# Kernel optimization log

Measured on AMD Instinct MI355X. Metric: run time of the kernel, lower is better.

The kernel has to match this reference:

```python
import jax, jax.numpy as jnp
import numpy as np

B, T, D, H = 2, 2048, 768, 12
HD = D // H  # head_dim = 64


def setup_inputs() -> dict:
    key = jax.random.key(0)
    ks = jax.random.split(key, 10)
    s = 0.02
    return {
        "hidden_states": jax.random.normal(ks[0], (B, T, D), jnp.float32),
        "attention_mask": jnp.zeros((B, 1, T, T), jnp.float32),
        "relative_position_bias": jax.random.normal(ks[1], (H, T, T), jnp.float32) * s,
        "Wq": jax.random.normal(ks[2], (D, D), jnp.float32) * s,
        "bq": jnp.zeros((D,), jnp.float32),
        "Wk": jax.random.normal(ks[3], (D, D), jnp.float32) * s,
        "bk": jnp.zeros((D,), jnp.float32),
        "Wv": jax.random.normal(ks[4], (D, D), jnp.float32) * s,
        "bv": jnp.zeros((D,), jnp.float32),
        "Wo": jax.random.normal(ks[5], (D, D), jnp.float32) * s,
        "bo": jnp.zeros((D,), jnp.float32),
    }


def reference(hidden_states, attention_mask, relative_position_bias,
              Wq, bq, Wk, bk, Wv, bv, Wo, bo):
    b, t, d = hidden_states.shape
    scale = HD ** -0.5
    # projections (nn.Linear: x @ W^T + b)
    q = (hidden_states @ Wq.T + bq) * scale
    k = hidden_states @ Wk.T + bk
    v = hidden_states @ Wv.T + bv
    # [b, h, t, hd]
    q = q.reshape(b, t, H, HD).transpose(0, 2, 1, 3)
    k = k.reshape(b, t, H, HD).transpose(0, 2, 1, 3)
    v = v.reshape(b, t, H, HD).transpose(0, 2, 1, 3)
    # scores: [b, h, t, s]
    attn = jnp.einsum("bhtd,bhsd->bhts", q, k)
    attn = attn + relative_position_bias[None, :, :, :]
    attn = attn + attention_mask  # (b,1,t,s) broadcast over heads
    attn = jax.nn.softmax(attn, axis=-1)
    out = jnp.einsum("bhts,bhsd->bhtd", attn, v)
    out = out.transpose(0, 2, 1, 3).reshape(b, t, d)
    return out @ Wo.T + bo
```

## Files before the change

kernel.cpp:

```cpp
#include <hip/hip_runtime.h>
#include <hip/hip_bf16.h>

#define B_  2
#define T_  2048
#define D_  768
#define H_  12
#define HD_ 64

typedef short bf16x8 __attribute__((ext_vector_type(8)));
typedef float f32x4  __attribute__((ext_vector_type(4)));

static __device__ __forceinline__ unsigned short f2bf(float f) {
    union { float f; unsigned u; } v; v.f = f;
    unsigned r = (v.u + 0x7FFFu + ((v.u >> 16) & 1u)) >> 16;
    return (unsigned short)r;
}

__global__ void cvt_f32_bf16(const float* __restrict__ in,
                             unsigned short* __restrict__ out, int n8) {
    int i = blockIdx.x * blockDim.x + threadIdx.x;
    int stride = gridDim.x * blockDim.x;
    for (; i < n8; i += stride) {
        float4 a = *(const float4*)(in + (size_t)i * 8);
        float4 b = *(const float4*)(in + (size_t)i * 8 + 4);
        union { unsigned short s[8]; int4 v; } o;
        o.s[0] = f2bf(a.x); o.s[1] = f2bf(a.y); o.s[2] = f2bf(a.z); o.s[3] = f2bf(a.w);
        o.s[4] = f2bf(b.x); o.s[5] = f2bf(b.y); o.s[6] = f2bf(b.z); o.s[7] = f2bf(b.w);
        *(int4*)(out + (size_t)i * 8) = o.v;
    }
}

__global__ __launch_bounds__(256)
void gemm_bt_bf16(const unsigned short* __restrict__ A,
                  const unsigned short* __restrict__ Bw,
                  const float* __restrict__ bias,
                  void* __restrict__ out, float scale, int mode)
{
    __shared__ __align__(16) unsigned short As[128 * 40];
    __shared__ __align__(16) unsigned short Bs[128 * 40];

    const int tid  = threadIdx.x;
    const int lane = tid & 63;
    const int wid  = tid >> 6;
    const int wm   = wid >> 1, wn = wid & 1;
    const int l15  = lane & 15, l16 = lane >> 4;
    const int bm   = blockIdx.x * 128, bn = blockIdx.y * 128;

    f32x4 acc[4][4];
    #pragma unroll
    for (int mi = 0; mi < 4; ++mi)
        #pragma unroll
        for (int ni = 0; ni < 4; ++ni)
            acc[mi][ni] = (f32x4){0.f, 0.f, 0.f, 0.f};

    const int r0 = tid >> 2,          o0 = (tid & 3) * 8;
    const int r1 = (tid + 256) >> 2,  o1 = ((tid + 256) & 3) * 8;

    for (int k0 = 0; k0 < 768; k0 += 32) {
        int4 a0 = *(const int4*)(A  + (size_t)(bm + r0) * 768 + k0 + o0);
        int4 a1 = *(const int4*)(A  + (size_t)(bm + r1) * 768 + k0 + o1);
        int4 b0 = *(const int4*)(Bw + (size_t)(bn + r0) * 768 + k0 + o0);
        int4 b1 = *(const int4*)(Bw + (size_t)(bn + r1) * 768 + k0 + o1);
        *(int4*)(As + r0 * 40 + o0) = a0;
        *(int4*)(As + r1 * 40 + o1) = a1;
        *(int4*)(Bs + r0 * 40 + o0) = b0;
        *(int4*)(Bs + r1 * 40 + o1) = b1;
        __syncthreads();

        bf16x8 af[4], bf[4];
        #pragma unroll
        for (int mi = 0; mi < 4; ++mi)
            af[mi] = *(const bf16x8*)(As + (wm * 64 + mi * 16 + l15) * 40 + l16 * 8);
        #pragma unroll
        for (int ni = 0; ni < 4; ++ni)
            bf[ni] = *(const bf16x8*)(Bs + (wn * 64 + ni * 16 + l15) * 40 + l16 * 8);
        #pragma unroll
        for (int mi = 0; mi < 4; ++mi)
            #pragma unroll
            for (int ni = 0; ni < 4; ++ni)
                acc[mi][ni] = __builtin_amdgcn_mfma_f32_16x16x32_bf16(
                    af[mi], bf[ni], acc[mi][ni], 0, 0, 0);
        __syncthreads();
    }

    if (mode == 0) {
        float* o = (float*)out;
        #pragma unroll
        for (int ni = 0; ni < 4; ++ni) {
            int col = bn + wn * 64 + ni * 16 + l15;
            float bv = bias[col];
            #pragma unroll
            for (int mi = 0; mi < 4; ++mi)
                #pragma unroll
                for (int reg = 0; reg < 4; ++reg) {
                    int row = bm + wm * 64 + mi * 16 + l16 * 4 + reg;
                    o[(size_t)row * 768 + col] = acc[mi][ni][reg] + bv;
                }
        }
    } else {
        unsigned short* o = (unsigned short*)out;
        #pragma unroll
        for (int ni = 0; ni < 4; ++ni) {
            int col = bn + wn * 64 + ni * 16 + l15;
            float bv = bias[col];
            int h = col >> 6, hd = col & 63;
            #pragma unroll
            for (int mi = 0; mi < 4; ++mi)
                #pragma unroll
                for (int reg = 0; reg < 4; ++reg) {
                    int row = bm + wm * 64 + mi * 16 + l16 * 4 + reg;
                    int bb = row >> 11, t = row & (T_ - 1);
                    float v = (acc[mi][ni][reg] + bv) * scale;
                    o[(((size_t)bb * H_ + h) * T_ + t) * HD_ + hd] = f2bf(v);
                }
        }
    }
}

__global__ __launch_bounds__(256)
void attn_fwd_mfma(const unsigned short* __restrict__ q,
                   const unsigned short* __restrict__ k,
                   const unsigned short* __restrict__ v,
                   const float* __restrict__ bias,
                   const float* __restrict__ mask,
                   unsigned short* __restrict__ ctx)
{
    __shared__ __align__(16) unsigned short Ks[64 * 72];
    __shared__ __align__(16) unsigned short Vt[64 * 72];
    __shared__ __align__(16) unsigned short Ps[64 * 72];

    const int tid  = threadIdx.x;
    const int lane = tid & 63;
    const int wq   = tid >> 6;
    const int l15  = lane & 15, l16 = lane >> 4;
    const int bh   = blockIdx.y;
    const int b    = bh / H_, h = bh % H_;
    const int q0   = blockIdx.x * 64;

    const unsigned short* qb = q + (size_t)bh * T_ * HD_;
    const unsigned short* kb = k + (size_t)bh * T_ * HD_;
    const unsigned short* vb = v + (size_t)bh * T_ * HD_;

    bf16x8 qf[2];
    {
        const unsigned short* qp = qb + (size_t)(q0 + wq * 16 + l15) * HD_;
        qf[0] = *(const bf16x8*)(qp + l16 * 8);
        qf[1] = *(const bf16x8*)(qp + 32 + l16 * 8);
    }

    float m_run[4], l_run[4];
    f32x4 o[4];
    #pragma unroll
    for (int r = 0; r < 4; ++r) {
        m_run[r] = -3.0e38f; l_run[r] = 0.f;
        o[r] = (f32x4){0.f, 0.f, 0.f, 0.f};
    }

    const size_t brow = (size_t)h * T_ * T_ + (size_t)(q0 + wq * 16) * T_;
    const size_t mrow = (size_t)b * T_ * T_ + (size_t)(q0 + wq * 16) * T_;

    for (int s0 = 0; s0 < T_; s0 += 64) {
        #pragma unroll
        for (int it = 0; it < 2; ++it) {
            int slot = tid + it * 256;
            int row = slot >> 3, c8 = (slot & 7) * 8;
            int4 kv = *(const int4*)(kb + (size_t)(s0 + row) * HD_ + c8);
            *(int4*)(Ks + row * 72 + c8) = kv;
            int key = slot & 63, hd0 = (slot >> 6) * 8;
            int4 vv = *(const int4*)(vb + (size_t)(s0 + key) * HD_ + hd0);
            const unsigned short* vs = (const unsigned short*)&vv;
            #pragma unroll
            for (int e = 0; e < 8; ++e)
                Vt[(hd0 + e) * 72 + key] = vs[e];
        }
        __syncthreads();

        float badd[4][4];
        #pragma unroll
        for (int f = 0; f < 4; ++f)
            #pragma unroll
            for (int reg = 0; reg < 4; ++reg) {
                size_t off = (size_t)(l16 * 4 + reg) * T_ + s0 + f * 16 + l15;
                badd[f][reg] = bias[brow + off] + mask[mrow + off];
            }

        f32x4 s[4];
        #pragma unroll
        for (int f = 0; f < 4; ++f) {
            bf16x8 k0f = *(const bf16x8*)(Ks + (f * 16 + l15) * 72 + l16 * 8);
            bf16x8 k1f = *(const bf16x8*)(Ks + (f * 16 + l15) * 72 + 32 + l16 * 8);
            f32x4 t = (f32x4){0.f, 0.f, 0.f, 0.f};
            t = __builtin_amdgcn_mfma_f32_16x16x32_bf16(qf[0], k0f, t, 0, 0, 0);
            t = __builtin_amdgcn_mfma_f32_16x16x32_bf16(qf[1], k1f, t, 0, 0, 0);
            s[f] = t;
        }

        #pragma unroll
        for (int f = 0; f < 4; ++f)
            #pragma unroll
            for (int reg = 0; reg < 4; ++reg)
                s[f][reg] += badd[f][reg];

        float sc[4];
        #pragma unroll
        for (int reg = 0; reg < 4; ++reg) {
            float mx = fmaxf(fmaxf(s[0][reg], s[1][reg]), fmaxf(s[2][reg], s[3][reg]));
            #pragma unroll
            for (int off = 1; off < 16; off <<= 1)
                mx = fmaxf(mx, __shfl_xor(mx, off));
            float m_new = fmaxf(m_run[reg], mx);
            float scv = __expf(m_run[reg] - m_new);
            float ssum = 0.f;
            #pragma unroll
            for (int f = 0; f < 4; ++f) {
                float p = __expf(s[f][reg] - m_new);
                s[f][reg] = p; ssum += p;
            }
            #pragma unroll
            for (int off = 1; off < 16; off <<= 1)
                ssum += __shfl_xor(ssum, off);
            l_run[reg] = l_run[reg] * scv + ssum;
            m_run[reg] = m_new;
            sc[reg] = scv;
        }
        #pragma unroll
        for (int f = 0; f < 4; ++f)
            #pragma unroll
            for (int reg = 0; reg < 4; ++reg)
                o[f][reg] *= sc[reg];

        unsigned short* Pw = Ps + wq * 16 * 72;
        #pragma unroll
        for (int f = 0; f < 4; ++f)
            #pragma unroll
            for (int reg = 0; reg < 4; ++reg)
                Pw[(l16 * 4 + reg) * 72 + f * 16 + l15] = f2bf(s[f][reg]);

        #pragma unroll
        for (int kc = 0; kc < 2; ++kc) {
            bf16x8 pf = *(const bf16x8*)(Pw + l15 * 72 + kc * 32 + l16 * 8);
            #pragma unroll
            for (int f = 0; f < 4; ++f) {
                bf16x8 vf = *(const bf16x8*)(Vt + (f * 16 + l15) * 72 + kc * 32 + l16 * 8);
                o[f] = __builtin_amdgcn_mfma_f32_16x16x32_bf16(pf, vf, o[f], 0, 0, 0);
            }
        }
        __syncthreads();
    }

    unsigned short* cb = ctx + ((size_t)b * T_ + q0 + wq * 16) * D_ + h * HD_;
    #pragma unroll
    for (int reg = 0; reg < 4; ++reg) {
        float inv = 1.f / l_run[reg];
        int r = l16 * 4 + reg;
        #pragma unroll
        for (int f = 0; f < 4; ++f)
            cb[(size_t)r * D_ + f * 16 + l15] = f2bf(o[f][reg] * inv);
    }
}

extern "C" void kernel_launch(void* const* d_in, const int* in_sizes, int n_in,
                              void* d_out, int out_size, void* d_ws, size_t ws_size,
                              hipStream_t stream) {
    const float* hs   = (const float*)d_in[0];
    const float* mask = (const float*)d_in[1];
    const float* bias = (const float*)d_in[2];
    const float* Wq   = (const float*)d_in[3];
    const float* bq   = (const float*)d_in[4];
    const float* Wk   = (const float*)d_in[5];
    const float* bk   = (const float*)d_in[6];
    const float* Wv   = (const float*)d_in[7];
    const float* bv   = (const float*)d_in[8];
    const float* Wo   = (const float*)d_in[9];
    const float* bo   = (const float*)d_in[10];
    float* out = (float*)d_out;

    const size_t NE = (size_t)B_ * T_ * D_;
    const size_t WE = (size_t)D_ * D_;
    unsigned short* ws = (unsigned short*)d_ws;
    unsigned short* hs_bf = ws;
    unsigned short* Wq_bf = hs_bf + NE;
    unsigned short* Wk_bf = Wq_bf + WE;
    unsigned short* Wv_bf = Wk_bf + WE;
    unsigned short* Wo_bf = Wv_bf + WE;
    unsigned short* qw    = Wo_bf + WE;
    unsigned short* kw    = qw + NE;
    unsigned short* vw    = kw + NE;
    unsigned short* ctxb  = vw + NE;

    {
        int n8 = (int)(NE / 8);
        cvt_f32_bf16<<<dim3((n8 + 255) / 256 > 2048 ? 2048 : (n8 + 255) / 256), 256, 0, stream>>>(hs, hs_bf, n8);
        int w8 = (int)(WE / 8);
        dim3 wg((w8 + 255) / 256);
        cvt_f32_bf16<<<wg, 256, 0, stream>>>(Wq, Wq_bf, w8);
        cvt_f32_bf16<<<wg, 256, 0, stream>>>(Wk, Wk_bf, w8);
        cvt_f32_bf16<<<wg, 256, 0, stream>>>(Wv, Wv_bf, w8);
        cvt_f32_bf16<<<wg, 256, 0, stream>>>(Wo, Wo_bf, w8);
    }

    dim3 ggrid(32, 6);
    const float scale = 0.125f;
    gemm_bt_bf16<<<ggrid, 256, 0, stream>>>(hs_bf, Wq_bf, bq, qw, scale, 1);
    gemm_bt_bf16<<<ggrid, 256, 0, stream>>>(hs_bf, Wk_bf, bk, kw, 1.0f, 1);
    gemm_bt_bf16<<<ggrid, 256, 0, stream>>>(hs_bf, Wv_bf, bv, vw, 1.0f, 1);

    attn_fwd_mfma<<<dim3(T_ / 64, B_ * H_), 256, 0, stream>>>(qw, kw, vw, bias, mask, ctxb);

    gemm_bt_bf16<<<ggrid, 256, 0, stream>>>(ctxb, Wo_bf, bo, out, 1.0f, 0);
}
```

Before: 479.6 us.

## Fuse QKV GEMMs, batch weight casts, use direct-to-LDS loads, transpose score layout

```diff
diff --git a/kernel.cpp b/kernel.cpp
--- a/kernel.cpp
+++ b/kernel.cpp
@@ -1,5 +1,4 @@
 #include <hip/hip_runtime.h>
-#include <hip/hip_bf16.h>
 
 #define B_  2
 #define T_  2048
@@ -9,6 +8,7 @@
 
 typedef short bf16x8 __attribute__((ext_vector_type(8)));
 typedef float f32x4  __attribute__((ext_vector_type(4)));
+typedef unsigned int u32;
 
 static __device__ __forceinline__ unsigned short f2bf(float f) {
     union { float f; unsigned u; } v; v.f = f;
@@ -30,80 +30,96 @@
     }
 }
 
+__global__ void cvt_weights(const float* __restrict__ w0, const float* __restrict__ w1,
+                            const float* __restrict__ w2, const float* __restrict__ w3,
+                            unsigned short* __restrict__ out, int n8) {
+    const float* src = (blockIdx.y == 0) ? w0 : (blockIdx.y == 1) ? w1
+                     : (blockIdx.y == 2) ? w2 : w3;
+    unsigned short* dst = out + (size_t)blockIdx.y * (D_ * D_);
+    int i = blockIdx.x * blockDim.x + threadIdx.x;
+    int stride = gridDim.x * blockDim.x;
+    for (; i < n8; i += stride) {
+        float4 a = *(const float4*)(src + (size_t)i * 8);
+        float4 b = *(const float4*)(src + (size_t)i * 8 + 4);
+        union { unsigned short s[8]; int4 v; } o;
+        o.s[0] = f2bf(a.x); o.s[1] = f2bf(a.y); o.s[2] = f2bf(a.z); o.s[3] = f2bf(a.w);
+        o.s[4] = f2bf(b.x); o.s[5] = f2bf(b.y); o.s[6] = f2bf(b.z); o.s[7] = f2bf(b.w);
+        *(int4*)(dst + (size_t)i * 8) = o.v;
+    }
+}
+
 __global__ __launch_bounds__(256)
-void gemm_bt_bf16(const unsigned short* __restrict__ A,
-                  const unsigned short* __restrict__ Bw,
-                  const float* __restrict__ bias,
-                  void* __restrict__ out, float scale, int mode)
+void gemm_bt_lds(const unsigned short* __restrict__ A,
+                 const unsigned short* __restrict__ W,
+                 const float* __restrict__ b0, const float* __restrict__ b1,
+                 const float* __restrict__ b2,
+                 void* __restrict__ outp, int mode)
 {
-    __shared__ __align__(16) unsigned short As[128 * 40];
-    __shared__ __align__(16) unsigned short Bs[128 * 40];
+    __shared__ __align__(16) unsigned short As[128 * 32];
+    __shared__ __align__(16) unsigned short Bs[64 * 32];
 
     const int tid  = threadIdx.x;
     const int lane = tid & 63;
     const int wid  = tid >> 6;
     const int wm   = wid >> 1, wn = wid & 1;
     const int l15  = lane & 15, l16 = lane >> 4;
-    const int bm   = blockIdx.x * 128, bn = blockIdx.y * 128;
-
-    f32x4 acc[4][4];
+    const int bm   = blockIdx.x * 128, bn = blockIdx.y * 64;
+
+    f32x4 acc[4][2];
     #pragma unroll
     for (int mi = 0; mi < 4; ++mi)
         #pragma unroll
-        for (int ni = 0; ni < 4; ++ni)
+        for (int ni = 0; ni < 2; ++ni)
             acc[mi][ni] = (f32x4){0.f, 0.f, 0.f, 0.f};
 
-    const int r0 = tid >> 2,          o0 = (tid & 3) * 8;
-    const int r1 = (tid + 256) >> 2,  o1 = ((tid + 256) & 3) * 8;
+    const int srow = lane >> 2;
+    const int scol = (lane & 3) * 8;
 
     for (int k0 = 0; k0 < 768; k0 += 32) {
-        int4 a0 = *(const int4*)(A  + (size_t)(bm + r0) * 768 + k0 + o0);
-        int4 a1 = *(const int4*)(A  + (size_t)(bm + r1) * 768 + k0 + o1);
-        int4 b0 = *(const int4*)(Bw + (size_t)(bn + r0) * 768 + k0 + o0);
-        int4 b1 = *(const int4*)(Bw + (size_t)(bn + r1) * 768 + k0 + o1);
-        *(int4*)(As + r0 * 40 + o0) = a0;
-        *(int4*)(As + r1 * 40 + o1) = a1;
-        *(int4*)(Bs + r0 * 40 + o0) = b0;
-        *(int4*)(Bs + r1 * 40 + o1) = b1;
+        #pragma unroll
+        for (int j = 0; j < 3; ++j) {
+            int c = wid * 3 + j;
+            const unsigned short* src;
+            unsigned short* dst;
+            if (c < 8) {
+                src = A + (size_t)(bm + c * 16 + srow) * 768 + k0 + scol;
+                dst = As + c * 512;
+            } else {
+                src = W + (size_t)(bn + (c - 8) * 16 + srow) * 768 + k0 + scol;
+                dst = Bs + (c - 8) * 512;
+            }
+            __builtin_amdgcn_global_load_lds(
+                (const __attribute__((address_space(1))) u32*)src,
+                (__attribute__((address_space(3))) u32*)dst, 16, 0, 0);
+        }
         __syncthreads();
 
-        bf16x8 af[4], bf[4];
+        bf16x8 af[4], bfr[2];
         #pragma unroll
         for (int mi = 0; mi < 4; ++mi)
-            af[mi] = *(const bf16x8*)(As + (wm * 64 + mi * 16 + l15) * 40 + l16 * 8);
-        #pragma unroll
-        for (int ni = 0; ni < 4; ++ni)
-            bf[ni] = *(const bf16x8*)(Bs + (wn * 64 + ni * 16 + l15) * 40 + l16 * 8);
+            af[mi] = *(const bf16x8*)(As + (wm * 64 + mi * 16 + l15) * 32 + l16 * 8);
+        #pragma unroll
+        for (int ni = 0; ni < 2; ++ni)
+            bfr[ni] = *(const bf16x8*)(Bs + (wn * 32 + ni * 16 + l15) * 32 + l16 * 8);
         #pragma unroll
         for (int mi = 0; mi < 4; ++mi)
             #pragma unroll
-            for (int ni = 0; ni < 4; ++ni)
+            for (int ni = 0; ni < 2; ++ni)
                 acc[mi][ni] = __builtin_amdgcn_mfma_f32_16x16x32_bf16(
-                    af[mi], bf[ni], acc[mi][ni], 0, 0, 0);
+                    af[mi], bfr[ni], acc[mi][ni], 0, 0, 0);
         __syncthreads();
     }
 
-    if (mode == 0) {
-        float* o = (float*)out;
-        #pragma unroll
-        for (int ni = 0; ni < 4; ++ni) {
-            int col = bn + wn * 64 + ni * 16 + l15;
-            float bv = bias[col];
-            #pragma unroll
-            for (int mi = 0; mi < 4; ++mi)
-                #pragma unroll
-                for (int reg = 0; reg < 4; ++reg) {
-                    int row = bm + wm * 64 + mi * 16 + l16 * 4 + reg;
-                    o[(size_t)row * 768 + col] = acc[mi][ni][reg] + bv;
-                }
-        }
-    } else {
-        unsigned short* o = (unsigned short*)out;
-        #pragma unroll
-        for (int ni = 0; ni < 4; ++ni) {
-            int col = bn + wn * 64 + ni * 16 + l15;
-            float bv = bias[col];
-            int h = col >> 6, hd = col & 63;
+    if (mode == 1) {
+        const int sel = bn / 768;
+        const float* bp = (sel == 0) ? b0 : (sel == 1) ? b1 : b2;
+        const float scale = (sel == 0) ? 0.125f : 1.0f;
+        unsigned short* o = (unsigned short*)outp + (size_t)sel * (B_ * T_ * D_);
+        #pragma unroll
+        for (int ni = 0; ni < 2; ++ni) {
+            int cg = bn - sel * 768 + wn * 32 + ni * 16 + l15;
+            float bv = bp[cg];
+            int h = cg >> 6, hd = cg & 63;
             #pragma unroll
             for (int mi = 0; mi < 4; ++mi)
                 #pragma unroll
@@ -112,6 +128,20 @@
                     int bb = row >> 11, t = row & (T_ - 1);
                     float v = (acc[mi][ni][reg] + bv) * scale;
                     o[(((size_t)bb * H_ + h) * T_ + t) * HD_ + hd] = f2bf(v);
+                }
+        }
+    } else {
+        float* o = (float*)outp;
+        #pragma unroll
+        for (int ni = 0; ni < 2; ++ni) {
+            int col = bn + wn * 32 + ni * 16 + l15;
+            float bv = b0[col];
+            #pragma unroll
+            for (int mi = 0; mi < 4; ++mi)
+                #pragma unroll
+                for (int reg = 0; reg < 4; ++reg) {
+                    int row = bm + wm * 64 + mi * 16 + l16 * 4 + reg;
+                    o[(size_t)row * 768 + col] = acc[mi][ni][reg] + bv;
                 }
         }
     }
@@ -148,16 +178,13 @@
         qf[1] = *(const bf16x8*)(qp + 32 + l16 * 8);
     }
 
-    float m_run[4], l_run[4];
+    float m_run = -3.0e38f, l_run = 0.f;
     f32x4 o[4];
     #pragma unroll
-    for (int r = 0; r < 4; ++r) {
-        m_run[r] = -3.0e38f; l_run[r] = 0.f;
-        o[r] = (f32x4){0.f, 0.f, 0.f, 0.f};
-    }
-
-    const size_t brow = (size_t)h * T_ * T_ + (size_t)(q0 + wq * 16) * T_;
-    const size_t mrow = (size_t)b * T_ * T_ + (size_t)(q0 + wq * 16) * T_;
+    for (int f = 0; f < 4; ++f) o[f] = (f32x4){0.f, 0.f, 0.f, 0.f};
+
+    const size_t brow = (size_t)h * T_ * T_ + (size_t)(q0 + wq * 16 + l15) * T_;
+    const size_t mrow = (size_t)b * T_ * T_ + (size_t)(q0 + wq * 16 + l15) * T_;
 
     for (int s0 = 0; s0 < T_; s0 += 64) {
         #pragma unroll
@@ -173,16 +200,14 @@
             for (int e = 0; e < 8; ++e)
                 Vt[(hd0 + e) * 72 + key] = vs[e];
         }
+
+        float4 bv4[4], mv4[4];
+        #pragma unroll
+        for (int f = 0; f < 4; ++f) {
+            bv4[f] = *(const float4*)(bias + brow + s0 + f * 16 + l16 * 4);
+            mv4[f] = *(const float4*)(mask + mrow + s0 + f * 16 + l16 * 4);
+        }
         __syncthreads();
-
-        float badd[4][4];
-        #pragma unroll
-        for (int f = 0; f < 4; ++f)
-            #pragma unroll
-            for (int reg = 0; reg < 4; ++reg) {
-                size_t off = (size_t)(l16 * 4 + reg) * T_ + s0 + f * 16 + l15;
-                badd[f][reg] = bias[brow + off] + mask[mrow + off];
-            }
 
         f32x4 s[4];
         #pragma unroll
@@ -190,51 +215,60 @@
             bf16x8 k0f = *(const bf16x8*)(Ks + (f * 16 + l15) * 72 + l16 * 8);
             bf16x8 k1f = *(const bf16x8*)(Ks + (f * 16 + l15) * 72 + 32 + l16 * 8);
             f32x4 t = (f32x4){0.f, 0.f, 0.f, 0.f};
-            t = __builtin_amdgcn_mfma_f32_16x16x32_bf16(qf[0], k0f, t, 0, 0, 0);
-            t = __builtin_amdgcn_mfma_f32_16x16x32_bf16(qf[1], k1f, t, 0, 0, 0);
+            t = __builtin_amdgcn_mfma_f32_16x16x32_bf16(k0f, qf[0], t, 0, 0, 0);
+            t = __builtin_amdgcn_mfma_f32_16x16x32_bf16(k1f, qf[1], t, 0, 0, 0);
             s[f] = t;
         }
 
         #pragma unroll
+        for (int f = 0; f < 4; ++f) {
+            const float* pb = (const float*)&bv4[f];
+            const float* pm = (const float*)&mv4[f];
+            #pragma unroll
+            for (int reg = 0; reg < 4; ++reg)
+                s[f][reg] += pb[reg] + pm[reg];
+        }
+
+        float mx = s[0][0];
+        #pragma unroll
         for (int f = 0; f < 4; ++f)
             #pragma unroll
             for (int reg = 0; reg < 4; ++reg)
-                s[f][reg] += badd[f][reg];
-
-        float sc[4];
-        #pragma unroll
-        for (int reg = 0; reg < 4; ++reg) {
-            float mx = fmaxf(fmaxf(s[0][reg], s[1][reg]), fmaxf(s[2][reg], s[3][reg]));
-            #pragma unroll
-            for (int off = 1; off < 16; off <<= 1)
-                mx = fmaxf(mx, __shfl_xor(mx, off));
-            float m_new = fmaxf(m_run[reg], mx);
-            float scv = __expf(m_run[reg] - m_new);
-            float ssum = 0.f;
-            #pragma unroll
-            for (int f = 0; f < 4; ++f) {
+                mx = fmaxf(mx, s[f][reg]);
+        mx = fmaxf(mx, __shfl_xor(mx, 16));
+        mx = fmaxf(mx, __shfl_xor(mx, 32));
+        float m_new = fmaxf(m_run, mx);
+        float scv = __expf(m_run - m_new);
+        float psum = 0.f;
+        #pragma unroll
+        for (int f = 0; f < 4; ++f)
+            #pragma unroll
+            for (int reg = 0; reg < 4; ++reg) {
                 float p = __expf(s[f][reg] - m_new);
-                s[f][reg] = p; ssum += p;
+                s[f][reg] = p; psum += p;
             }
-            #pragma unroll
-            for (int off = 1; off < 16; off <<= 1)
-                ssum += __shfl_xor(ssum, off);
-            l_run[reg] = l_run[reg] * scv + ssum;
-            m_run[reg] = m_new;
-            sc[reg] = scv;
-        }
+        psum += __shfl_xor(psum, 16);
+        psum += __shfl_xor(psum, 32);
+        l_run = l_run * scv + psum;
+        m_run = m_new;
+
+        float scq[4];
+        #pragma unroll
+        for (int reg = 0; reg < 4; ++reg) scq[reg] = __shfl(scv, l16 * 4 + reg);
         #pragma unroll
         for (int f = 0; f < 4; ++f)
             #pragma unroll
             for (int reg = 0; reg < 4; ++reg)
-                o[f][reg] *= sc[reg];
+                o[f][reg] *= scq[reg];
 
         unsigned short* Pw = Ps + wq * 16 * 72;
         #pragma unroll
-        for (int f = 0; f < 4; ++f)
-            #pragma unroll
-            for (int reg = 0; reg < 4; ++reg)
-                Pw[(l16 * 4 + reg) * 72 + f * 16 + l15] = f2bf(s[f][reg]);
+        for (int f = 0; f < 4; ++f) {
+            ushort4 pk;
+            pk.x = f2bf(s[f][0]); pk.y = f2bf(s[f][1]);
+            pk.z = f2bf(s[f][2]); pk.w = f2bf(s[f][3]);
+            *(ushort4*)(Pw + l15 * 72 + f * 16 + l16 * 4) = pk;
+        }
 
         #pragma unroll
         for (int kc = 0; kc < 2; ++kc) {
@@ -248,14 +282,17 @@
         __syncthreads();
     }
 
-    unsigned short* cb = ctx + ((size_t)b * T_ + q0 + wq * 16) * D_ + h * HD_;
+    float linv[4];
+    #pragma unroll
+    for (int reg = 0; reg < 4; ++reg)
+        linv[reg] = 1.0f / __shfl(l_run, l16 * 4 + reg);
     #pragma unroll
     for (int reg = 0; reg < 4; ++reg) {
-        float inv = 1.f / l_run[reg];
-        int r = l16 * 4 + reg;
+        int t = q0 + wq * 16 + l16 * 4 + reg;
+        unsigned short* cb = ctx + ((size_t)b * T_ + t) * D_ + h * HD_;
         #pragma unroll
         for (int f = 0; f < 4; ++f)
-            cb[(size_t)r * D_ + f * 16 + l15] = f2bf(o[f][reg] * inv);
+            cb[f * 16 + l15] = f2bf(o[f][reg] * linv[reg]);
     }
 }
 
@@ -279,33 +316,17 @@
     const size_t WE = (size_t)D_ * D_;
     unsigned short* ws = (unsigned short*)d_ws;
     unsigned short* hs_bf = ws;
-    unsigned short* Wq_bf = hs_bf + NE;
-    unsigned short* Wk_bf = Wq_bf + WE;
-    unsigned short* Wv_bf = Wk_bf + WE;
-    unsigned short* Wo_bf = Wv_bf + WE;
-    unsigned short* qw    = Wo_bf + WE;
-    unsigned short* kw    = qw + NE;
-    unsigned short* vw    = kw + NE;
-    unsigned short* ctxb  = vw + NE;
-
-    {
-        int n8 = (int)(NE / 8);
-        cvt_f32_bf16<<<dim3((n8 + 255) / 256 > 2048 ? 2048 : (n8 + 255) / 256), 256, 0, stream>>>(hs, hs_bf, n8);
-        int w8 = (int)(WE / 8);
-        dim3 wg((w8 + 255) / 256);
-        cvt_f32_bf16<<<wg, 256, 0, stream>>>(Wq, Wq_bf, w8);
-        cvt_f32_bf16<<<wg, 256, 0, stream>>>(Wk, Wk_bf, w8);
-        cvt_f32_bf16<<<wg, 256, 0, stream>>>(Wv, Wv_bf, w8);
-        cvt_f32_bf16<<<wg, 256, 0, stream>>>(Wo, Wo_bf, w8);
-    }
-
-    dim3 ggrid(32, 6);
-    const float scale = 0.125f;
-    gemm_bt_bf16<<<ggrid, 256, 0, stream>>>(hs_bf, Wq_bf, bq, qw, scale, 1);
-    gemm_bt_bf16<<<ggrid, 256, 0, stream>>>(hs_bf, Wk_bf, bk, kw, 1.0f, 1);
-    gemm_bt_bf16<<<ggrid, 256, 0, stream>>>(hs_bf, Wv_bf, bv, vw, 1.0f, 1);
-
-    attn_fwd_mfma<<<dim3(T_ / 64, B_ * H_), 256, 0, stream>>>(qw, kw, vw, bias, mask, ctxb);
-
-    gemm_bt_bf16<<<ggrid, 256, 0, stream>>>(ctxb, Wo_bf, bo, out, 1.0f, 0);
-}
+    unsigned short* wbf   = hs_bf + NE;
+    unsigned short* qkv   = wbf + 4 * WE;
+    unsigned short* ctxb  = qkv + 3 * NE;
+
+    cvt_f32_bf16<<<dim3(1536), 256, 0, stream>>>(hs, hs_bf, (int)(NE / 8));
+    cvt_weights<<<dim3(288, 4), 256, 0, stream>>>(Wq, Wk, Wv, Wo, wbf, (int)(WE / 8));
+
+    gemm_bt_lds<<<dim3(32, 36), 256, 0, stream>>>(hs_bf, wbf, bq, bk, bv, qkv, 1);
+
+    attn_fwd_mfma<<<dim3(T_ / 64, B_ * H_), 256, 0, stream>>>(
+        qkv, qkv + NE, qkv + 2 * NE, bias, mask, ctxb);
+
+    gemm_bt_lds<<<dim3(32, 12), 256, 0, stream>>>(ctxb, wbf + 3 * WE, bo, nullptr, nullptr, out, 0);
+}
```

Result: no change. 477.0 us (-0.5%).
